# Optimization experiments

Hardware: AMD Instinct MI355X
Metric: run time of the kernel (lower is better)

Reference implementation:

```python
import jax, jax.numpy as jnp
import numpy as np

B, S, E, H = 2, 2048, 1024, 16
D = E // H
THETA = 10000.0


def _rope_cos_sin():
    # Faithful to source: freqs_cis is indexed by input_shape[1], which after
    # _split_heads is the HEAD dimension, so 'positions' are head indices 0..H-1.
    freqs = 1.0 / (THETA ** (jnp.arange(0, D, 2, dtype=jnp.float32) / D))  # [D/2]
    pos = jnp.arange(H, dtype=jnp.float32)  # head indices (source bug, reproduced)
    ang = jnp.outer(pos, freqs)  # [H, D/2]
    # broadcast shape [1, H, 1, D/2] against [B, H, S, D/2]
    return jnp.cos(ang)[None, :, None, :], jnp.sin(ang)[None, :, None, :]


def _apply_rope(x, cos, sin):
    # x: [B, H, S, D]; complex pairs are (even, odd) along last dim
    xe, xo = x[..., 0::2], x[..., 1::2]
    re = xe * cos - xo * sin
    im = xe * sin + xo * cos
    # interleave back: view_as_real(...).flatten(3)
    return jnp.stack([re, im], axis=-1).reshape(x.shape)


def setup_inputs() -> dict:
    key = jax.random.key(0)
    ks = jax.random.split(key, 5)
    s = 0.02
    return {
        "hidden_states": jax.random.normal(ks[0], (B, S, E), dtype=jnp.float32),
        "W_attn": jax.random.normal(ks[1], (E, 3 * E), dtype=jnp.float32) * s,
        "b_attn": jnp.zeros((3 * E,), dtype=jnp.float32),
        "W_proj": jax.random.normal(ks[2], (E, E), dtype=jnp.float32) * s,
        "b_proj": jnp.zeros((E,), dtype=jnp.float32),
    }


def reference(hidden_states, W_attn, b_attn, W_proj, b_proj):
    qkv = hidden_states @ W_attn + b_attn  # [B, S, 3E]
    q, k, v = jnp.split(qkv, 3, axis=-1)
    # split heads -> [B, H, S, D]
    def split_heads(t):
        return t.reshape(B, S, H, D).transpose(0, 2, 1, 3)
    q, k, v = split_heads(q), split_heads(k), split_heads(v)
    cos, sin = _rope_cos_sin()
    q = _apply_rope(q, cos, sin)
    k = _apply_rope(k, cos, sin)
    scores = jnp.einsum("bhqd,bhkd->bhqk", q, k) / jnp.sqrt(jnp.float32(D))
    causal = jnp.tril(jnp.ones((S, S), dtype=bool))
    neg = jnp.finfo(scores.dtype).min
    scores = jnp.where(causal[None, None], scores, neg)
    attn = jax.nn.softmax(scores, axis=-1)
    out = jnp.einsum("bhqk,bhkd->bhqd", attn, v)  # [B, H, S, D]
    out = out.transpose(0, 2, 1, 3).reshape(B, S, E)  # merge heads
    return out @ W_proj + b_proj
```

## Files before the change

kernel.cpp:

```cpp
#include <hip/hip_runtime.h>
#include <hip/hip_bf16.h>
#include <cstdint>
#include <cstddef>


typedef float  f32x4 __attribute__((ext_vector_type(4)));
typedef __bf16 bf16x8 __attribute__((ext_vector_type(8)));

__device__ __forceinline__ unsigned short f2bf(float f) {
  union { __bf16 b; unsigned short u; } c; c.b = (__bf16)f; return c.u;
}
__device__ __forceinline__ unsigned short bf2u(__bf16 b) {
  union { __bf16 b; unsigned short u; } c; c.b = b; return c.u;
}

__device__ __forceinline__ void gload_lds16(const void* g, void* l) {
  __builtin_amdgcn_global_load_lds(
      (const __attribute__((address_space(1))) unsigned int*)g,
      (__attribute__((address_space(3))) unsigned int*)l, 16, 0, 0);
}

__global__ __launch_bounds__(256) void cast_x_k(const float* __restrict__ in,
                                                __bf16* __restrict__ out) {
  size_t i = (size_t)blockIdx.x * 256 + threadIdx.x;
  f32x4 a = *(const f32x4*)(in + i * 8);
  f32x4 b = *(const f32x4*)(in + i * 8 + 4);
  bf16x8 o;
  o[0]=(__bf16)a[0]; o[1]=(__bf16)a[1]; o[2]=(__bf16)a[2]; o[3]=(__bf16)a[3];
  o[4]=(__bf16)b[0]; o[5]=(__bf16)b[1]; o[6]=(__bf16)b[2]; o[7]=(__bf16)b[3];
  *(bf16x8*)(out + i * 8) = o;
}

template<bool ROPE>
__global__ __launch_bounds__(256) void transpose_rot_k(const float* __restrict__ W,
                                                       __bf16* __restrict__ Wt,
                                                       int Kd, int Nd) {
  __shared__ float tile[32][33];
  const int tx = threadIdx.x, ty = threadIdx.y;
  const int n0 = blockIdx.x * 32, k0 = blockIdx.y * 32;
#pragma unroll
  for (int i = 0; i < 4; i++)
    tile[ty + 8 * i][tx] = W[(size_t)(k0 + ty + 8 * i) * Nd + n0 + tx];
  __syncthreads();
#pragma unroll
  for (int i = 0; i < 4; i++) {
    int nl = ty + 8 * i;
    int n  = n0 + nl;
    float v;
    if (ROPE && n < 2048) {
      int nn = n & 1023;
      int h = nn >> 6, d = nn & 63, ip = d >> 1;
      float ang = (float)h * powf(10000.0f, -(float)ip / 32.0f);
      float s, c; sincosf(ang, &s, &c);
      float xe = tile[tx][nl & ~1], xo = tile[tx][nl | 1];
      v = (d & 1) ? (xe * s + xo * c) : (xe * c - xo * s);
    } else {
      v = tile[tx][nl];
    }
    Wt[(size_t)n * Kd + k0 + tx] = (__bf16)v;
  }
}

__global__ __launch_bounds__(256) void rot_bias_k(const float* __restrict__ b,
                                                  float* __restrict__ out) {
  int n = blockIdx.x * 256 + threadIdx.x;
  if (n < 3072) {
    float v;
    if (n < 2048) {
      int nn = n & 1023, h = nn >> 6, d = nn & 63, ip = d >> 1;
      float ang = (float)h * powf(10000.0f, -(float)ip / 32.0f);
      float s, c; sincosf(ang, &s, &c);
      float xe = b[n & ~1], xo = b[n | 1];
      v = (d & 1) ? (xe * s + xo * c) : (xe * c - xo * s);
    } else v = b[n];
    out[n] = v;
  }
}

template<int MODE>
__global__ __launch_bounds__(256) void gemm_bt_k(
    const __bf16* __restrict__ A, const __bf16* __restrict__ Bt,
    const float* __restrict__ bias, float* __restrict__ outf,
    __bf16* __restrict__ Qo, __bf16* __restrict__ Ko, __bf16* __restrict__ Vo,
    int M, int N, int K)
{
  __shared__ __align__(16) char Asm[8192];
  __shared__ __align__(16) char Bsm[8192];
  const int tid = threadIdx.x;
  const int m0 = blockIdx.y * 128, n0 = blockIdx.x * 128;
  const int wid = tid >> 6, lane = tid & 63;
  const int wr = wid >> 1, wc = wid & 1;
  const int li = lane & 15, gq = lane >> 4;

  const f32x4 fzero = {0.f, 0.f, 0.f, 0.f};
  f32x4 acc[4][4];
#pragma unroll
  for (int i = 0; i < 4; i++)
#pragma unroll
    for (int j = 0; j < 4; j++) acc[i][j] = fzero;

  const int NT = K >> 5;

  for (int kt = 0; kt < NT; ++kt) {
    const int ko = kt * 32;
#pragma unroll
    for (int it = 0; it < 2; it++) {
      const int idx = wid * 128 + it * 64 + lane;
      const int row = idx >> 2, cb = idx & 3;
      char* la = Asm + (size_t)(wid * 128 + it * 64) * 16;
      char* lb = Bsm + (size_t)(wid * 128 + it * 64) * 16;
      gload_lds16(A  + (size_t)(m0 + row) * K + ko + cb * 8, la);
      gload_lds16(Bt + (size_t)(n0 + row) * K + ko + cb * 8, lb);
    }
    __syncthreads();
    bf16x8 af[4], bfr[4];
#pragma unroll
    for (int mi = 0; mi < 4; mi++)
      af[mi] = *(const bf16x8*)(Asm + (wr * 64 + mi * 16 + li) * 64 + gq * 16);
#pragma unroll
    for (int ni = 0; ni < 4; ni++)
      bfr[ni] = *(const bf16x8*)(Bsm + (wc * 64 + ni * 16 + li) * 64 + gq * 16);
#pragma unroll
    for (int mi = 0; mi < 4; mi++)
#pragma unroll
      for (int ni = 0; ni < 4; ni++)
        acc[mi][ni] = __builtin_amdgcn_mfma_f32_16x16x32_bf16(af[mi], bfr[ni],
                                                              acc[mi][ni], 0, 0, 0);
    __syncthreads();
  }

#pragma unroll
  for (int ni = 0; ni < 4; ni++) {
    const int n = n0 + wc * 64 + ni * 16 + li;
    const float bv = bias[n];
#pragma unroll
    for (int mi = 0; mi < 4; mi++) {
#pragma unroll
      for (int r = 0; r < 4; r++) {
        const int m = m0 + wr * 64 + mi * 16 + 4 * gq + r;
        const float val = acc[mi][ni][r] + bv;
        if (MODE == 0) {
          const int region = n >> 10, nn = n & 1023;
          const int h = nn >> 6, d = nn & 63;
          const int b = m >> 11, s = m & 2047;
          __bf16* dst = (region == 0) ? Qo : (region == 1) ? Ko : Vo;
          dst[(((size_t)(b * 16 + h)) * 2048 + s) * 64 + d] = (__bf16)val;
        } else {
          outf[(size_t)m * N + n] = val;
        }
      }
    }
  }
}

__global__ __launch_bounds__(512) void attn_k(
    const __bf16* __restrict__ Q, const __bf16* __restrict__ K,
    const __bf16* __restrict__ V, __bf16* __restrict__ O)
{
  __shared__ __align__(16) char Ksm[2][8192];
  __shared__ __align__(16) char Vsm[2][8192];
  __shared__ __align__(16) char Psm[8][2048];
  const int qt = blockIdx.x, bh = blockIdx.y;
  const int tid = threadIdx.x, wid = tid >> 6, lane = tid & 63;
  const int li = lane & 15, gq = lane >> 4;
  const size_t base = (size_t)bh * 2048 * 64;
  const int iq = qt * 128 + wid * 16 + li;
  const int wkmax = qt * 128 + wid * 16 + 15;
  const int swz = (li & 7) << 4;
  const f32x4 fzero = {0.f, 0.f, 0.f, 0.f};
  const int ktmax = 2 * qt + 1;

  bf16x8 qf[2];
#pragma unroll
  for (int kc = 0; kc < 2; kc++)
    qf[kc] = *(const bf16x8*)(Q + base + (size_t)iq * 64 + kc * 32 + gq * 8);

  f32x4 o[4];
#pragma unroll
  for (int dn = 0; dn < 4; dn++) o[dn] = fzero;
  float mrun = -1e30f, lrun = 0.f;
  char* pw = Psm[wid];

  const bool roleK = (wid < 4);
  const int st = tid & 255;
  const int krow0 = st >> 3, kcb = st & 7;
  const int krow1 = krow0 + 32;
  const int vkk = (st >> 3) * 2, vd0 = (st & 7) * 8;
  f32x4 kreg0, kreg1;
  bf16x8 vreg0, vreg1;

  auto loadTile = [&](int kt) {
    if (roleK) {
      kreg0 = *(const f32x4*)(K + base + (size_t)(kt * 64 + krow0) * 64 + kcb * 8);
      kreg1 = *(const f32x4*)(K + base + (size_t)(kt * 64 + krow1) * 64 + kcb * 8);
    } else {
      vreg0 = *(const bf16x8*)(V + base + (size_t)(kt * 64 + vkk)     * 64 + vd0);
      vreg1 = *(const bf16x8*)(V + base + (size_t)(kt * 64 + vkk + 1) * 64 + vd0);
    }
  };
  auto writeTile = [&](int buf) {
    if (roleK) {
      *(f32x4*)(Ksm[buf] + ((krow0 * 128 + kcb * 16) ^ ((krow0 & 7) << 4))) = kreg0;
      *(f32x4*)(Ksm[buf] + ((krow1 * 128 + kcb * 16) ^ ((krow1 & 7) << 4))) = kreg1;
    } else {
#pragma unroll
      for (int j = 0; j < 8; j++) {
        int d = vd0 + j;
        unsigned w = (unsigned)bf2u(vreg0[j]) | ((unsigned)bf2u(vreg1[j]) << 16);
        *(unsigned*)(Vsm[buf] + ((d * 128 + vkk * 2) ^ ((d & 7) << 4))) = w;
      }
    }
  };

  loadTile(0);
  writeTile(0);
  __syncthreads();
  int cur = 0;

  for (int kt = 0; kt <= ktmax; ++kt) {
    if (kt < ktmax) loadTile(kt + 1);

    if (kt * 64 <= wkmax) {
      f32x4 s4[4];
#pragma unroll
      for (int f = 0; f < 4; f++) s4[f] = fzero;
#pragma unroll
      for (int kc = 0; kc < 2; kc++) {
#pragma unroll
        for (int f = 0; f < 4; f++) {
          bf16x8 kf = *(const bf16x8*)(Ksm[cur] +
              (((f * 16 + li) * 128 + kc * 64 + gq * 16) ^ swz));
          s4[f] = __builtin_amdgcn_mfma_f32_16x16x32_bf16(kf, qf[kc], s4[f], 0, 0, 0);
        }
      }
      float p[4][4];
      float tmax = -1e30f;
#pragma unroll
      for (int f = 0; f < 4; f++)
#pragma unroll
        for (int r = 0; r < 4; r++) {
          float sv = s4[f][r] * 0.125f;
          int j = kt * 64 + f * 16 + 4 * gq + r;
          if (j > iq) sv = -1e30f;
          p[f][r] = sv;
          tmax = fmaxf(tmax, sv);
        }
      tmax = fmaxf(tmax, __shfl_xor(tmax, 16));
      tmax = fmaxf(tmax, __shfl_xor(tmax, 32));
      float mnew  = fmaxf(mrun, tmax);
      float alpha = __expf(mrun - mnew);
      mrun = mnew;
      float ts = 0.f;
#pragma unroll
      for (int f = 0; f < 4; f++)
#pragma unroll
        for (int r = 0; r < 4; r++) {
          float pv = __expf(p[f][r] - mnew);
          p[f][r] = pv;
          ts += pv;
        }
      ts += __shfl_xor(ts, 16);
      ts += __shfl_xor(ts, 32);
      lrun = lrun * alpha + ts;
#pragma unroll
      for (int r = 0; r < 4; r++) {
        float ar = __shfl(alpha, 4 * gq + r);
#pragma unroll
        for (int dn = 0; dn < 4; dn++) o[dn][r] *= ar;
      }
#pragma unroll
      for (int f = 0; f < 4; f++) {
        unsigned lo = (unsigned)f2bf(p[f][0]) | ((unsigned)f2bf(p[f][1]) << 16);
        unsigned hi = (unsigned)f2bf(p[f][2]) | ((unsigned)f2bf(p[f][3]) << 16);
        uint2 w2; w2.x = lo; w2.y = hi;
        *(uint2*)(pw + ((li * 128 + f * 32 + gq * 8) ^ swz)) = w2;
      }
#pragma unroll
      for (int kc = 0; kc < 2; kc++) {
        bf16x8 paf = *(const bf16x8*)(pw + ((li * 128 + kc * 64 + gq * 16) ^ swz));
#pragma unroll
        for (int dn = 0; dn < 4; dn++) {
          bf16x8 vb = *(const bf16x8*)(Vsm[cur] +
              (((dn * 16 + li) * 128 + kc * 64 + gq * 16) ^ swz));
          o[dn] = __builtin_amdgcn_mfma_f32_16x16x32_bf16(paf, vb, o[dn], 0, 0, 0);
        }
      }
    }

    if (kt < ktmax) {
      __syncthreads();
      writeTile(cur ^ 1);
      __syncthreads();
      cur ^= 1;
    }
  }

  const int b = bh >> 4, h = bh & 15;
#pragma unroll
  for (int r = 0; r < 4; r++) {
    float lr  = __shfl(lrun, 4 * gq + r);
    float inv = 1.0f / lr;
    int qrow = qt * 128 + wid * 16 + 4 * gq + r;
#pragma unroll
    for (int dn = 0; dn < 4; dn++) {
      O[((size_t)(b * 2048 + qrow)) * 1024 + h * 64 + dn * 16 + li] =
          (__bf16)(o[dn][r] * inv);
    }
  }
}

extern "C" void kernel_launch(void* const* d_in, const int* in_sizes, int n_in,
                              void* d_out, int out_size, void* d_ws, size_t ws_size,
                              hipStream_t stream) {
  const float* hidden = (const float*)d_in[0];
  const float* W_attn = (const float*)d_in[1];
  const float* b_attn = (const float*)d_in[2];
  const float* W_proj = (const float*)d_in[3];
  const float* b_proj = (const float*)d_in[4];
  float* out = (float*)d_out;

  char* ws = (char*)d_ws;
  size_t off = 0;
  auto alloc = [&](size_t bytes) -> char* {
    char* p = ws + off;
    off += (bytes + 255) & ~(size_t)255;
    return p;
  };
  __bf16* Xb  = (__bf16*)alloc((size_t)4096 * 1024 * 2);
  __bf16* Wat = (__bf16*)alloc((size_t)3072 * 1024 * 2);
  __bf16* Wpt = (__bf16*)alloc((size_t)1024 * 1024 * 2);
  float*  ba  = (float*) alloc((size_t)3072 * 4);
  __bf16* Qb  = (__bf16*)alloc((size_t)32 * 2048 * 64 * 2);
  __bf16* Kb  = (__bf16*)alloc((size_t)32 * 2048 * 64 * 2);
  __bf16* Vb  = (__bf16*)alloc((size_t)32 * 2048 * 64 * 2);
  __bf16* Ob  = (__bf16*)alloc((size_t)4096 * 1024 * 2);

  cast_x_k<<<2048, 256, 0, stream>>>(hidden, Xb);
  transpose_rot_k<true ><<<dim3(96, 32), dim3(32, 8), 0, stream>>>(W_attn, Wat, 1024, 3072);
  transpose_rot_k<false><<<dim3(32, 32), dim3(32, 8), 0, stream>>>(W_proj, Wpt, 1024, 1024);
  rot_bias_k<<<12, 256, 0, stream>>>(b_attn, ba);

  gemm_bt_k<0><<<dim3(24, 32), 256, 0, stream>>>(Xb, Wat, ba, nullptr,
                                                 Qb, Kb, Vb, 4096, 3072, 1024);
  attn_k<<<dim3(16, 32), 512, 0, stream>>>(Qb, Kb, Vb, Ob);
  gemm_bt_k<1><<<dim3(8, 32), 256, 0, stream>>>(Ob, Wpt, b_proj, out,
                                                nullptr, nullptr, nullptr,
                                                4096, 1024, 1024);
}
```

Before: 249.7 us.

## Double-buffer GEMMs, balance causal attention via paired query tiles, lazy softmax rescale

The GEMM kernel gains double-buffered LDS staging so the next K-slice load overlaps the MFMA work, and the output projection uses a 128x64 tile to launch more blocks. Attention now uses 256-thread blocks that each process a short and a long causal query tile (qt and 31-qt), which balances work across blocks. It also skips masking on off-diagonal tiles, folds the log2e factor into the scale so exp2f can be used, and rescales the running max only when it grows by more than a threshold. The lazy rescale and exp2 changes touch numerics, and the larger per-block register footprint may affect occupancy.

```diff
diff --git a/kernel.cpp b/kernel.cpp
--- a/kernel.cpp
+++ b/kernel.cpp
@@ -77,56 +77,77 @@
   }
 }
 
-template<int MODE>
+template<int MODE, int BN>
 __global__ __launch_bounds__(256) void gemm_bt_k(
     const __bf16* __restrict__ A, const __bf16* __restrict__ Bt,
     const float* __restrict__ bias, float* __restrict__ outf,
     __bf16* __restrict__ Qo, __bf16* __restrict__ Ko, __bf16* __restrict__ Vo,
     int M, int N, int K)
 {
-  __shared__ __align__(16) char Asm[8192];
-  __shared__ __align__(16) char Bsm[8192];
+  constexpr int MI = (BN == 128) ? 4 : 2;
+  __shared__ __align__(16) char Asm[2][8192];
+  __shared__ __align__(16) char Bsm[2][BN * 64];
   const int tid = threadIdx.x;
-  const int m0 = blockIdx.y * 128, n0 = blockIdx.x * 128;
+  const int m0 = blockIdx.y * 128, n0 = blockIdx.x * BN;
   const int wid = tid >> 6, lane = tid & 63;
-  const int wr = wid >> 1, wc = wid & 1;
+  const int wr = (BN == 128) ? (wid >> 1) : wid;
+  const int wc = (BN == 128) ? (wid & 1) : 0;
   const int li = lane & 15, gq = lane >> 4;
 
   const f32x4 fzero = {0.f, 0.f, 0.f, 0.f};
-  f32x4 acc[4][4];
-#pragma unroll
-  for (int i = 0; i < 4; i++)
+  f32x4 acc[MI][4];
+#pragma unroll
+  for (int i = 0; i < MI; i++)
 #pragma unroll
     for (int j = 0; j < 4; j++) acc[i][j] = fzero;
 
   const int NT = K >> 5;
 
-  for (int kt = 0; kt < NT; ++kt) {
+  auto stage = [&](int buf, int kt) {
     const int ko = kt * 32;
 #pragma unroll
     for (int it = 0; it < 2; it++) {
       const int idx = wid * 128 + it * 64 + lane;
       const int row = idx >> 2, cb = idx & 3;
-      char* la = Asm + (size_t)(wid * 128 + it * 64) * 16;
-      char* lb = Bsm + (size_t)(wid * 128 + it * 64) * 16;
-      gload_lds16(A  + (size_t)(m0 + row) * K + ko + cb * 8, la);
-      gload_lds16(Bt + (size_t)(n0 + row) * K + ko + cb * 8, lb);
-    }
-    __syncthreads();
-    bf16x8 af[4], bfr[4];
-#pragma unroll
-    for (int mi = 0; mi < 4; mi++)
-      af[mi] = *(const bf16x8*)(Asm + (wr * 64 + mi * 16 + li) * 64 + gq * 16);
+      gload_lds16(A + (size_t)(m0 + row) * K + ko + cb * 8,
+                  Asm[buf] + (size_t)(wid * 128 + it * 64) * 16);
+    }
+    if constexpr (BN == 128) {
+#pragma unroll
+      for (int it = 0; it < 2; it++) {
+        const int idx = wid * 128 + it * 64 + lane;
+        const int row = idx >> 2, cb = idx & 3;
+        gload_lds16(Bt + (size_t)(n0 + row) * K + ko + cb * 8,
+                    Bsm[buf] + (size_t)(wid * 128 + it * 64) * 16);
+      }
+    } else {
+      const int row = tid >> 2, cb = tid & 3;
+      gload_lds16(Bt + (size_t)(n0 + row) * K + ko + cb * 8,
+                  Bsm[buf] + (size_t)(wid * 64) * 16);
+    }
+  };
+
+  stage(0, 0);
+  __syncthreads();
+  int cur = 0;
+
+  for (int kt = 0; kt < NT; ++kt) {
+    if (kt + 1 < NT) stage(cur ^ 1, kt + 1);
+    bf16x8 af[MI], bfr[4];
+#pragma unroll
+    for (int mi = 0; mi < MI; mi++)
+      af[mi] = *(const bf16x8*)(Asm[cur] + (wr * (MI * 16) + mi * 16 + li) * 64 + gq * 16);
 #pragma unroll
     for (int ni = 0; ni < 4; ni++)
-      bfr[ni] = *(const bf16x8*)(Bsm + (wc * 64 + ni * 16 + li) * 64 + gq * 16);
-#pragma unroll
-    for (int mi = 0; mi < 4; mi++)
+      bfr[ni] = *(const bf16x8*)(Bsm[cur] + (wc * 64 + ni * 16 + li) * 64 + gq * 16);
+#pragma unroll
+    for (int mi = 0; mi < MI; mi++)
 #pragma unroll
       for (int ni = 0; ni < 4; ni++)
         acc[mi][ni] = __builtin_amdgcn_mfma_f32_16x16x32_bf16(af[mi], bfr[ni],
                                                               acc[mi][ni], 0, 0, 0);
     __syncthreads();
+    cur ^= 1;
   }
 
 #pragma unroll
@@ -134,10 +155,10 @@
     const int n = n0 + wc * 64 + ni * 16 + li;
     const float bv = bias[n];
 #pragma unroll
-    for (int mi = 0; mi < 4; mi++) {
+    for (int mi = 0; mi < MI; mi++) {
 #pragma unroll
       for (int r = 0; r < 4; r++) {
-        const int m = m0 + wr * 64 + mi * 16 + 4 * gq + r;
+        const int m = m0 + wr * (MI * 16) + mi * 16 + 4 * gq + r;
         const float val = acc[mi][ni][r] + bv;
         if (MODE == 0) {
           const int region = n >> 10, nn = n & 1023;
@@ -153,160 +174,202 @@
   }
 }
 
-__global__ __launch_bounds__(512) void attn_k(
+__global__ __launch_bounds__(256) void attn_k(
     const __bf16* __restrict__ Q, const __bf16* __restrict__ K,
     const __bf16* __restrict__ V, __bf16* __restrict__ O)
 {
   __shared__ __align__(16) char Ksm[2][8192];
   __shared__ __align__(16) char Vsm[2][8192];
-  __shared__ __align__(16) char Psm[8][2048];
-  const int qt = blockIdx.x, bh = blockIdx.y;
+  __shared__ __align__(16) char Psm[4][2048];
+  const int pr = blockIdx.x, bh = blockIdx.y;
+  const int qta = pr, qtb = 31 - pr;
+  const int NTa = qta + 1;
+  const int NT  = NTa + qtb + 1;
   const int tid = threadIdx.x, wid = tid >> 6, lane = tid & 63;
   const int li = lane & 15, gq = lane >> 4;
   const size_t base = (size_t)bh * 2048 * 64;
-  const int iq = qt * 128 + wid * 16 + li;
-  const int wkmax = qt * 128 + wid * 16 + 15;
   const int swz = (li & 7) << 4;
   const f32x4 fzero = {0.f, 0.f, 0.f, 0.f};
-  const int ktmax = 2 * qt + 1;
-
-  bf16x8 qf[2];
-#pragma unroll
-  for (int kc = 0; kc < 2; kc++)
-    qf[kc] = *(const bf16x8*)(Q + base + (size_t)iq * 64 + kc * 32 + gq * 8);
+  const float SC = 0.18033688011f;
+
+  const int rowa = qta * 64 + wid * 16 + li;
+  const int rowb = qtb * 64 + wid * 16 + li;
+  bf16x8 qfa[2], qfb[2], qcur[2];
+#pragma unroll
+  for (int kc = 0; kc < 2; kc++) {
+    qfa[kc] = *(const bf16x8*)(Q + base + (size_t)rowa * 64 + kc * 32 + gq * 8);
+    qfb[kc] = *(const bf16x8*)(Q + base + (size_t)rowb * 64 + kc * 32 + gq * 8);
+  }
+  qcur[0] = qfa[0]; qcur[1] = qfa[1];
 
   f32x4 o[4];
 #pragma unroll
   for (int dn = 0; dn < 4; dn++) o[dn] = fzero;
   float mrun = -1e30f, lrun = 0.f;
+  int iq = rowa;
   char* pw = Psm[wid];
-
-  const bool roleK = (wid < 4);
-  const int st = tid & 255;
-  const int krow0 = st >> 3, kcb = st & 7;
-  const int krow1 = krow0 + 32;
-  const int vkk = (st >> 3) * 2, vd0 = (st & 7) * 8;
-  f32x4 kreg0, kreg1;
-  bf16x8 vreg0, vreg1;
-
-  auto loadTile = [&](int kt) {
+  const int b = bh >> 4, h = bh & 15;
+
+  auto epilogue = [&](int qt) {
+#pragma unroll
+    for (int r = 0; r < 4; r++) {
+      float lr  = __shfl(lrun, 4 * gq + r);
+      float inv = 1.0f / lr;
+      int qrow = qt * 64 + wid * 16 + 4 * gq + r;
+#pragma unroll
+      for (int dn = 0; dn < 4; dn++) {
+        O[((size_t)(b * 2048 + qrow)) * 1024 + h * 64 + dn * 16 + li] =
+            (__bf16)(o[dn][r] * inv);
+      }
+    }
+  };
+
+  const bool roleK = (wid < 2);
+  const int st = tid & 127;
+  const int vkk = (st >> 3) * 4, vd0 = (st & 7) * 8;
+  f32x4 kreg[4];
+  bf16x8 vreg[4];
+
+  auto loadTile = [&](int ko) {
     if (roleK) {
-      kreg0 = *(const f32x4*)(K + base + (size_t)(kt * 64 + krow0) * 64 + kcb * 8);
-      kreg1 = *(const f32x4*)(K + base + (size_t)(kt * 64 + krow1) * 64 + kcb * 8);
+#pragma unroll
+      for (int t = 0; t < 4; t++) {
+        const int ci = st + 128 * t;
+        const int row = ci >> 3, cb = ci & 7;
+        kreg[t] = *(const f32x4*)(K + base + (size_t)(ko + row) * 64 + cb * 8);
+      }
     } else {
-      vreg0 = *(const bf16x8*)(V + base + (size_t)(kt * 64 + vkk)     * 64 + vd0);
-      vreg1 = *(const bf16x8*)(V + base + (size_t)(kt * 64 + vkk + 1) * 64 + vd0);
+#pragma unroll
+      for (int u = 0; u < 4; u++)
+        vreg[u] = *(const bf16x8*)(V + base + (size_t)(ko + vkk + u) * 64 + vd0);
     }
   };
   auto writeTile = [&](int buf) {
     if (roleK) {
-      *(f32x4*)(Ksm[buf] + ((krow0 * 128 + kcb * 16) ^ ((krow0 & 7) << 4))) = kreg0;
-      *(f32x4*)(Ksm[buf] + ((krow1 * 128 + kcb * 16) ^ ((krow1 & 7) << 4))) = kreg1;
+#pragma unroll
+      for (int t = 0; t < 4; t++) {
+        const int ci = st + 128 * t;
+        const int row = ci >> 3, cb = ci & 7;
+        *(f32x4*)(Ksm[buf] + ((row * 128 + cb * 16) ^ ((row & 7) << 4))) = kreg[t];
+      }
     } else {
 #pragma unroll
       for (int j = 0; j < 8; j++) {
-        int d = vd0 + j;
-        unsigned w = (unsigned)bf2u(vreg0[j]) | ((unsigned)bf2u(vreg1[j]) << 16);
-        *(unsigned*)(Vsm[buf] + ((d * 128 + vkk * 2) ^ ((d & 7) << 4))) = w;
+        const int d = vd0 + j;
+        uint2 w;
+        w.x = (unsigned)bf2u(vreg[0][j]) | ((unsigned)bf2u(vreg[1][j]) << 16);
+        w.y = (unsigned)bf2u(vreg[2][j]) | ((unsigned)bf2u(vreg[3][j]) << 16);
+        *(uint2*)(Vsm[buf] + ((d * 128 + vkk * 2) ^ ((d & 7) << 4))) = w;
       }
     }
   };
 
-  loadTile(0);
+  auto kofs = [&](int i) { return (i < NTa ? i : i - NTa) * 64; };
+
+  loadTile(kofs(0));
   writeTile(0);
+  loadTile(kofs(1));
   __syncthreads();
-  int cur = 0;
-
-  for (int kt = 0; kt <= ktmax; ++kt) {
-    if (kt < ktmax) loadTile(kt + 1);
-
-    if (kt * 64 <= wkmax) {
-      f32x4 s4[4];
-#pragma unroll
-      for (int f = 0; f < 4; f++) s4[f] = fzero;
-#pragma unroll
-      for (int kc = 0; kc < 2; kc++) {
-#pragma unroll
-        for (int f = 0; f < 4; f++) {
-          bf16x8 kf = *(const bf16x8*)(Ksm[cur] +
-              (((f * 16 + li) * 128 + kc * 64 + gq * 16) ^ swz));
-          s4[f] = __builtin_amdgcn_mfma_f32_16x16x32_bf16(kf, qf[kc], s4[f], 0, 0, 0);
-        }
-      }
-      float p[4][4];
-      float tmax = -1e30f;
+
+  for (int i = 0; i < NT; ++i) {
+    const int cur = i & 1;
+    if (i + 1 < NT) writeTile(cur ^ 1);
+    if (i + 2 < NT) loadTile(kofs(i + 2));
+
+    if (i == NTa) {
+      epilogue(qta);
+#pragma unroll
+      for (int dn = 0; dn < 4; dn++) o[dn] = fzero;
+      mrun = -1e30f; lrun = 0.f;
+      iq = rowb;
+      qcur[0] = qfb[0]; qcur[1] = qfb[1];
+    }
+    const bool diag = (i == NTa - 1) || (i == NT - 1);
+    const int kbase = kofs(i);
+
+    f32x4 s4[4];
+#pragma unroll
+    for (int f = 0; f < 4; f++) s4[f] = fzero;
+#pragma unroll
+    for (int kc = 0; kc < 2; kc++) {
+#pragma unroll
+      for (int f = 0; f < 4; f++) {
+        bf16x8 kf = *(const bf16x8*)(Ksm[cur] +
+            (((f * 16 + li) * 128 + kc * 64 + gq * 16) ^ swz));
+        s4[f] = __builtin_amdgcn_mfma_f32_16x16x32_bf16(kf, qcur[kc], s4[f], 0, 0, 0);
+      }
+    }
+    float p[4][4];
+    float tmax = -1e30f;
+    if (diag) {
 #pragma unroll
       for (int f = 0; f < 4; f++)
 #pragma unroll
         for (int r = 0; r < 4; r++) {
-          float sv = s4[f][r] * 0.125f;
-          int j = kt * 64 + f * 16 + 4 * gq + r;
+          float sv = s4[f][r] * SC;
+          int j = kbase + f * 16 + 4 * gq + r;
           if (j > iq) sv = -1e30f;
           p[f][r] = sv;
           tmax = fmaxf(tmax, sv);
         }
-      tmax = fmaxf(tmax, __shfl_xor(tmax, 16));
-      tmax = fmaxf(tmax, __shfl_xor(tmax, 32));
+    } else {
+#pragma unroll
+      for (int f = 0; f < 4; f++)
+#pragma unroll
+        for (int r = 0; r < 4; r++) {
+          float sv = s4[f][r] * SC;
+          p[f][r] = sv;
+          tmax = fmaxf(tmax, sv);
+        }
+    }
+    tmax = fmaxf(tmax, __shfl_xor(tmax, 16));
+    tmax = fmaxf(tmax, __shfl_xor(tmax, 32));
+    if (!__all(tmax - mrun <= 11.0f)) {
       float mnew  = fmaxf(mrun, tmax);
-      float alpha = __expf(mrun - mnew);
-      mrun = mnew;
-      float ts = 0.f;
-#pragma unroll
-      for (int f = 0; f < 4; f++)
-#pragma unroll
-        for (int r = 0; r < 4; r++) {
-          float pv = __expf(p[f][r] - mnew);
-          p[f][r] = pv;
-          ts += pv;
-        }
-      ts += __shfl_xor(ts, 16);
-      ts += __shfl_xor(ts, 32);
-      lrun = lrun * alpha + ts;
+      float alpha = exp2f(mrun - mnew);
 #pragma unroll
       for (int r = 0; r < 4; r++) {
         float ar = __shfl(alpha, 4 * gq + r);
 #pragma unroll
         for (int dn = 0; dn < 4; dn++) o[dn][r] *= ar;
       }
-#pragma unroll
-      for (int f = 0; f < 4; f++) {
-        unsigned lo = (unsigned)f2bf(p[f][0]) | ((unsigned)f2bf(p[f][1]) << 16);
-        unsigned hi = (unsigned)f2bf(p[f][2]) | ((unsigned)f2bf(p[f][3]) << 16);
-        uint2 w2; w2.x = lo; w2.y = hi;
-        *(uint2*)(pw + ((li * 128 + f * 32 + gq * 8) ^ swz)) = w2;
-      }
-#pragma unroll
-      for (int kc = 0; kc < 2; kc++) {
-        bf16x8 paf = *(const bf16x8*)(pw + ((li * 128 + kc * 64 + gq * 16) ^ swz));
-#pragma unroll
-        for (int dn = 0; dn < 4; dn++) {
-          bf16x8 vb = *(const bf16x8*)(Vsm[cur] +
-              (((dn * 16 + li) * 128 + kc * 64 + gq * 16) ^ swz));
-          o[dn] = __builtin_amdgcn_mfma_f32_16x16x32_bf16(paf, vb, o[dn], 0, 0, 0);
-        }
-      }
-    }
-
-    if (kt < ktmax) {
-      __syncthreads();
-      writeTile(cur ^ 1);
-      __syncthreads();
-      cur ^= 1;
-    }
-  }
-
-  const int b = bh >> 4, h = bh & 15;
-#pragma unroll
-  for (int r = 0; r < 4; r++) {
-    float lr  = __shfl(lrun, 4 * gq + r);
-    float inv = 1.0f / lr;
-    int qrow = qt * 128 + wid * 16 + 4 * gq + r;
-#pragma unroll
-    for (int dn = 0; dn < 4; dn++) {
-      O[((size_t)(b * 2048 + qrow)) * 1024 + h * 64 + dn * 16 + li] =
-          (__bf16)(o[dn][r] * inv);
-    }
-  }
+      lrun *= alpha;
+      mrun = mnew;
+    }
+    float ts = 0.f;
+#pragma unroll
+    for (int f = 0; f < 4; f++)
+#pragma unroll
+      for (int r = 0; r < 4; r++) {
+        float pv = exp2f(p[f][r] - mrun);
+        p[f][r] = pv;
+        ts += pv;
+      }
+    ts += __shfl_xor(ts, 16);
+    ts += __shfl_xor(ts, 32);
+    lrun += ts;
+#pragma unroll
+    for (int f = 0; f < 4; f++) {
+      unsigned lo = (unsigned)f2bf(p[f][0]) | ((unsigned)f2bf(p[f][1]) << 16);
+      unsigned hi = (unsigned)f2bf(p[f][2]) | ((unsigned)f2bf(p[f][3]) << 16);
+      uint2 w2; w2.x = lo; w2.y = hi;
+      *(uint2*)(pw + ((li * 128 + f * 32 + gq * 8) ^ swz)) = w2;
+    }
+#pragma unroll
+    for (int kc = 0; kc < 2; kc++) {
+      bf16x8 paf = *(const bf16x8*)(pw + ((li * 128 + kc * 64 + gq * 16) ^ swz));
+#pragma unroll
+      for (int dn = 0; dn < 4; dn++) {
+        bf16x8 vb = *(const bf16x8*)(Vsm[cur] +
+            (((dn * 16 + li) * 128 + kc * 64 + gq * 16) ^ swz));
+        o[dn] = __builtin_amdgcn_mfma_f32_16x16x32_bf16(paf, vb, o[dn], 0, 0, 0);
+      }
+    }
+
+    __syncthreads();
+  }
+
+  epilogue(qtb);
 }
 
 extern "C" void kernel_launch(void* const* d_in, const int* in_sizes, int n_in,
@@ -340,10 +403,10 @@
   transpose_rot_k<false><<<dim3(32, 32), dim3(32, 8), 0, stream>>>(W_proj, Wpt, 1024, 1024);
   rot_bias_k<<<12, 256, 0, stream>>>(b_attn, ba);
 
-  gemm_bt_k<0><<<dim3(24, 32), 256, 0, stream>>>(Xb, Wat, ba, nullptr,
-                                                 Qb, Kb, Vb, 4096, 3072, 1024);
-  attn_k<<<dim3(16, 32), 512, 0, stream>>>(Qb, Kb, Vb, Ob);
-  gemm_bt_k<1><<<dim3(8, 32), 256, 0, stream>>>(Ob, Wpt, b_proj, out,
-                                                nullptr, nullptr, nullptr,
-                                                4096, 1024, 1024);
-}
+  gemm_bt_k<0, 128><<<dim3(24, 32), 256, 0, stream>>>(Xb, Wat, ba, nullptr,
+                                                      Qb, Kb, Vb, 4096, 3072, 1024);
+  attn_k<<<dim3(16, 32), 256, 0, stream>>>(Qb, Kb, Vb, Ob);
+  gemm_bt_k<1, 64><<<dim3(16, 32), 256, 0, stream>>>(Ob, Wpt, b_proj, out,
+                                                     nullptr, nullptr, nullptr,
+                                                     4096, 1024, 1024);
+}
```

After: 219.8 us. 1.14x faster.
